# Optimization experiments

Hardware: AMD Instinct MI355X
Metric: run time of the kernel (lower is better)

## Reference

```python
import jax, jax.numpy as jnp
import numpy as np

MARGIN = 0.5
HIERARCHY_LEVEL = 0
EPS = 1e-05


def setup_inputs() -> dict:
    key = jax.random.key(0)
    k1, k2, k3, k4 = jax.random.split(key, 4)
    n, m, d, L, n_classes = 4096, 32768, 128, 2, 100
    embeddings = jax.random.normal(k1, (n, d), dtype=jnp.float32)
    ref_embeddings = jax.random.normal(k2, (m, d), dtype=jnp.float32)
    labels = jax.random.randint(k3, (n, L), 0, n_classes, dtype=jnp.int64)
    ref_labels = jax.random.randint(k4, (m, L), 0, n_classes, dtype=jnp.int64)
    return {"embeddings": embeddings, "labels": labels,
            "ref_embeddings": ref_embeddings, "ref_labels": ref_labels}


def reference(embeddings, labels, ref_embeddings, ref_labels):
    # select hierarchy level
    lab = labels[:, HIERARCHY_LEVEL]          # [n]
    ref_lab = ref_labels[:, HIERARCHY_LEVEL]  # [m]
    n = embeddings.shape[0]
    sim = embeddings @ ref_embeddings.T       # [n, m]
    same = lab[:, None] == ref_lab[None, :]   # [n, m] bool
    # positive pairs: same label and sim < 1 - eps -> contribute (1 - sim)
    pos_mask = same & (sim < 1.0 - EPS)
    # negative pairs: different label and sim > margin -> contribute sim
    neg_mask = (~same) & (sim > MARGIN)
    pos_loss = jnp.sum(jnp.where(pos_mask, 1.0 - sim, 0.0))
    neg_loss = jnp.sum(jnp.where(neg_mask, sim, 0.0))
    return (pos_loss + neg_loss) / n
```

## Files before the change

kernel.cpp:

```cpp
#include <hip/hip_runtime.h>
#include <stdint.h>

#define N_EMB 4096
#define M_REF 32768
#define D_K   128
#define BM    128
#define BN    64
#define NT_PER 16
#define COLCHUNK (BN * NT_PER)
#define NCCHUNK (M_REF / COLCHUNK)
#define NROWT  (N_EMB / BM)
#define XBLOCKS (NROWT * NCCHUNK)

typedef __attribute__((ext_vector_type(8))) short short8;
typedef __attribute__((ext_vector_type(4))) float float4v;

static __device__ __forceinline__ unsigned short f2bf(float f) {
    unsigned int u = __builtin_bit_cast(unsigned int, f);
    u += 0x7FFFu + ((u >> 16) & 1u);
    return (unsigned short)(u >> 16);
}

#define CVT_THREADS (768 * 256)

__global__ void cvt_kernel(const float* __restrict__ emb, const float* __restrict__ ref,
                           unsigned short* __restrict__ aw, unsigned short* __restrict__ bw,
                           float* __restrict__ out) {
    const int NA4 = N_EMB * D_K / 4;
    int i0 = blockIdx.x * 256 + threadIdx.x;
    if (i0 == 0) *out = 0.0f;
    #pragma unroll
    for (int k = 0; k < 6; ++k) {
        int i = i0 + k * CVT_THREADS;
        const float4* src;
        unsigned short* dst;
        int j;
        if (i < NA4) { src = (const float4*)emb; dst = aw; j = i; }
        else         { src = (const float4*)ref; dst = bw; j = i - NA4; }
        float4 v = src[j];
        ushort4 o;
        o.x = f2bf(v.x); o.y = f2bf(v.y); o.z = f2bf(v.z); o.w = f2bf(v.w);
        *(ushort4*)(dst + (size_t)j * 4) = o;
    }
}

static __device__ __forceinline__ void gld_lds16(const void* g, void* l) {
    __builtin_amdgcn_global_load_lds((__attribute__((address_space(1))) void*)g,
                                     (__attribute__((address_space(3))) void*)l,
                                     16, 0, 0);
}

template<int NI>
static __device__ __forceinline__ void stage_rows(const unsigned short* __restrict__ g,
                                                  unsigned short* l, int tid) {
    const int rlow = tid >> 4;
    const int sc   = (tid & 15) ^ rlow;
    const char* g0 = (const char*)g + (rlow * D_K + sc * 8) * 2;
    char* l0 = (char*)l + tid * 16;
    #pragma unroll
    for (int i = 0; i < NI; ++i)
        gld_lds16(g0 + (size_t)i * (16 * D_K * 2), l0 + i * 4096);
}

__launch_bounds__(256, 3)
__global__ void xbm_kernel(const unsigned short* __restrict__ aw,
                           const unsigned short* __restrict__ bw,
                           const int* __restrict__ lab,
                           const int* __restrict__ rlab,
                           float* __restrict__ out) {
    __shared__ unsigned short b_sm[2][BN * D_K];
    __shared__ float red_sm[4];

    const int tid  = threadIdx.x;
    const int lane = tid & 63;
    const int wave = tid >> 6;
    const int quad = lane >> 4;
    const int l15  = lane & 15;

    const int rtile  = blockIdx.x >> 5;
    const int cchunk = blockIdx.x & 31;
    const int row0 = rtile * BM;
    const int col0 = cchunk * COLCHUNK;

    stage_rows<8>(aw + (size_t)row0 * D_K, &b_sm[0][0], tid);

    int labv[2][4];
    #pragma unroll
    for (int mt = 0; mt < 2; ++mt)
        #pragma unroll
        for (int r = 0; r < 4; ++r)
            labv[mt][r] = lab[(row0 + wave * 32 + mt * 16 + quad * 4 + r) * 2];

    __syncthreads();

    short8 a_reg[2][4];
    #pragma unroll
    for (int mt = 0; mt < 2; ++mt) {
        int ml = wave * 32 + mt * 16 + l15;
        #pragma unroll
        for (int ks = 0; ks < 4; ++ks) {
            int cs = (ks * 4 + quad) ^ l15;
            a_reg[mt][ks] = *(const short8*)(&b_sm[0][0] + (size_t)ml * D_K + cs * 8);
        }
    }
    __syncthreads();

    stage_rows<4>(bw + (size_t)col0 * D_K, b_sm[0], tid);

    float lsum[4] = {0.0f, 0.0f, 0.0f, 0.0f};

    #define COMPUTE_TILE(BP, CBASE)                                               \
        {                                                                         \
            const unsigned short* bp_ = (BP);                                     \
            const int cb_ = (CBASE);                                              \
            int rl[4];                                                            \
            _Pragma("unroll")                                                     \
            for (int nt = 0; nt < 4; ++nt)                                        \
                rl[nt] = rlab[(cb_ + nt * 16 + l15) * 2];                         \
            float4v acc[2][4] = {};                                               \
            _Pragma("unroll")                                                     \
            for (int ks = 0; ks < 4; ++ks) {                                      \
                short8 breg[4];                                                   \
                _Pragma("unroll")                                                 \
                for (int nt = 0; nt < 4; ++nt) {                                  \
                    int nl = nt * 16 + l15;                                       \
                    int cs = (ks * 4 + quad) ^ l15;                               \
                    breg[nt] = *(const short8*)(bp_ + (size_t)nl * D_K + cs * 8); \
                }                                                                 \
                _Pragma("unroll")                                                 \
                for (int mt = 0; mt < 2; ++mt)                                    \
                    _Pragma("unroll")                                             \
                    for (int nt = 0; nt < 4; ++nt)                                \
                        acc[mt][nt] = __builtin_amdgcn_mfma_f32_16x16x32_bf16(    \
                            a_reg[mt][ks], breg[nt], acc[mt][nt], 0, 0, 0);       \
            }                                                                     \
            _Pragma("unroll")                                                     \
            for (int mt = 0; mt < 2; ++mt)                                        \
                _Pragma("unroll")                                                 \
                for (int nt = 0; nt < 4; ++nt)                                    \
                    _Pragma("unroll")                                             \
                    for (int r = 0; r < 4; ++r) {                                 \
                        float s = acc[mt][nt][r];                                 \
                               \
                        float pos = fmaxf(1.0f - s, 0.0f);                        \
                        float neg = (s > 0.5f) ? s : 0.0f;                        \
                        lsum[r] += (labv[mt][r] == rl[nt]) ? pos : neg;           \
                    }                                                             \
        }

    #pragma unroll 1
    for (int t = 0; t < NT_PER; t += 2) {
        __syncthreads();
        stage_rows<4>(bw + (size_t)(col0 + (t + 1) * BN) * D_K, b_sm[1], tid);
        COMPUTE_TILE(b_sm[0], col0 + t * BN);
        __syncthreads();
        if (t + 2 < NT_PER)
            stage_rows<4>(bw + (size_t)(col0 + (t + 2) * BN) * D_K, b_sm[0], tid);
        COMPUTE_TILE(b_sm[1], col0 + (t + 1) * BN);
    }

    float loss = (lsum[0] + lsum[1]) + (lsum[2] + lsum[3]);
    #pragma unroll
    for (int off = 32; off > 0; off >>= 1)
        loss += __shfl_down(loss, off, 64);
    if (lane == 0) red_sm[wave] = loss;
    __syncthreads();
    if (tid == 0) {
        float v = (red_sm[0] + red_sm[1] + red_sm[2] + red_sm[3]) * (1.0f / (float)N_EMB);
        atomicAdd(out, v);
    }
}

extern "C" void kernel_launch(void* const* d_in, const int* in_sizes, int n_in,
                              void* d_out, int out_size, void* d_ws, size_t ws_size,
                              hipStream_t stream) {
    const float* emb     = (const float*)d_in[0];
    const int*   labels  = (const int*)d_in[1];
    const float* ref     = (const float*)d_in[2];
    const int*   rlabels = (const int*)d_in[3];
    float* out = (float*)d_out;

    unsigned short* aw = (unsigned short*)d_ws;
    unsigned short* bw = aw + (size_t)N_EMB * D_K;

    cvt_kernel<<<768, 256, 0, stream>>>(emb, ref, aw, bw, out);
    xbm_kernel<<<XBLOCKS, 256, 0, stream>>>(aw, bw,
                                            (const int*)labels, (const int*)rlabels, out);
}
```

Baseline: 120.3 us.

## Restructure GEMM-loss kernel with 4-stage LDS ring and 8-wave 2x4 tiling

Moves to 512-thread blocks with a 2x4 wave grid, each wave holding 64 A rows in registers loaded straight from global memory. B tiles and their labels stream through a 4-deep LDS ring using async global-to-LDS loads with explicit vmcnt waits and raw barriers. Row labels are packed into bytes and MFMA bursts run at raised priority. Fewer, larger blocks with longer column chunks are meant to hide load latency and cut per-block overhead, at the cost of more LDS, tighter register budgets and fragile hand-tuned wait counts.

Measured after the change: 268.2 us. 2.23x slower.

```diff
diff --git a/kernel.cpp b/kernel.cpp
--- a/kernel.cpp
+++ b/kernel.cpp
@@ -6,11 +6,9 @@
 #define D_K   128
 #define BM    128
 #define BN    64
-#define NT_PER 16
-#define COLCHUNK (BN * NT_PER)
-#define NCCHUNK (M_REF / COLCHUNK)
-#define NROWT  (N_EMB / BM)
-#define XBLOCKS (NROWT * NCCHUNK)
+#define NT    32
+#define COLCHUNK (BN * NT)
+#define XBLOCKS ((N_EMB / BM) * (M_REF / COLCHUNK))
 
 typedef __attribute__((ext_vector_type(8))) short short8;
 typedef __attribute__((ext_vector_type(4))) float float4v;
@@ -49,115 +47,139 @@
                                      (__attribute__((address_space(3))) void*)l,
                                      16, 0, 0);
 }
-
-template<int NI>
-static __device__ __forceinline__ void stage_rows(const unsigned short* __restrict__ g,
-                                                  unsigned short* l, int tid) {
-    const int rlow = tid >> 4;
-    const int sc   = (tid & 15) ^ rlow;
-    const char* g0 = (const char*)g + (rlow * D_K + sc * 8) * 2;
-    char* l0 = (char*)l + tid * 16;
-    #pragma unroll
-    for (int i = 0; i < NI; ++i)
-        gld_lds16(g0 + (size_t)i * (16 * D_K * 2), l0 + i * 4096);
-}
-
-__launch_bounds__(256, 3)
+static __device__ __forceinline__ void gld_lds4(const void* g, void* l) {
+    __builtin_amdgcn_global_load_lds((__attribute__((address_space(1))) void*)g,
+                                     (__attribute__((address_space(3))) void*)l,
+                                     4, 0, 0);
+}
+
+#define WAITVM(N) asm volatile("s_waitcnt vmcnt(" #N ")" ::: "memory")
+#define FENCE()   asm volatile("" ::: "memory")
+
+__launch_bounds__(512, 4)
 __global__ void xbm_kernel(const unsigned short* __restrict__ aw,
                            const unsigned short* __restrict__ bw,
                            const int* __restrict__ lab,
                            const int* __restrict__ rlab,
                            float* __restrict__ out) {
-    __shared__ unsigned short b_sm[2][BN * D_K];
-    __shared__ float red_sm[4];
+    __shared__ __align__(16) unsigned short b_sm[4][BN * D_K];
+    __shared__ int lab_sm[4][BN];
+    __shared__ float red_sm[8];
 
     const int tid  = threadIdx.x;
     const int lane = tid & 63;
     const int wave = tid >> 6;
+    const int wm   = wave >> 2;
+    const int wn   = wave & 3;
     const int quad = lane >> 4;
     const int l15  = lane & 15;
 
-    const int rtile  = blockIdx.x >> 5;
-    const int cchunk = blockIdx.x & 31;
+    const int rtile  = blockIdx.x >> 4;
+    const int cchunk = blockIdx.x & 15;
     const int row0 = rtile * BM;
     const int col0 = cchunk * COLCHUNK;
 
-    stage_rows<8>(aw + (size_t)row0 * D_K, &b_sm[0][0], tid);
-
-    int labv[2][4];
-    #pragma unroll
-    for (int mt = 0; mt < 2; ++mt)
+    short8 a_reg[4][4];
+    #pragma unroll
+    for (int mt = 0; mt < 4; ++mt)
         #pragma unroll
-        for (int r = 0; r < 4; ++r)
-            labv[mt][r] = lab[(row0 + wave * 32 + mt * 16 + quad * 4 + r) * 2];
-
-    __syncthreads();
-
-    short8 a_reg[2][4];
-    #pragma unroll
-    for (int mt = 0; mt < 2; ++mt) {
-        int ml = wave * 32 + mt * 16 + l15;
-        #pragma unroll
-        for (int ks = 0; ks < 4; ++ks) {
-            int cs = (ks * 4 + quad) ^ l15;
-            a_reg[mt][ks] = *(const short8*)(&b_sm[0][0] + (size_t)ml * D_K + cs * 8);
+        for (int ks = 0; ks < 4; ++ks)
+            a_reg[mt][ks] = *(const short8*)(aw +
+                (size_t)(row0 + wm * 64 + mt * 16 + l15) * D_K + (ks * 4 + quad) * 8);
+
+    unsigned int labp[4];
+    #pragma unroll
+    for (int mt = 0; mt < 4; ++mt) {
+        int base = (row0 + wm * 64 + mt * 16 + quad * 4) * 2;
+        int4 p0 = *(const int4*)(lab + base);
+        int4 p1 = *(const int4*)(lab + base + 4);
+        labp[mt] = (unsigned)p0.x | ((unsigned)p0.z << 8) |
+                   ((unsigned)p1.x << 16) | ((unsigned)p1.z << 24);
+    }
+
+    #define STAGE(T, R)                                                          \
+        {                                                                        \
+            const char* g0_ = (const char*)(bw + (size_t)(col0 + (T) * BN) * D_K) + \
+                ((tid >> 4) * D_K + (((tid & 15) ^ ((tid >> 4) & 15)) * 8)) * 2; \
+            char* l0_ = (char*)&b_sm[R][0] + tid * 16;                           \
+            gld_lds16(g0_, l0_);                                                 \
+            gld_lds16(g0_ + 32 * 256, l0_ + 8192);                               \
+            gld_lds4(rlab + (size_t)(col0 + (T) * BN + lane) * 2,                \
+                     (char*)&lab_sm[R][0] + lane * 4);                           \
         }
-    }
-    __syncthreads();
-
-    stage_rows<4>(bw + (size_t)col0 * D_K, b_sm[0], tid);
+
+    FENCE();
+    STAGE(0, 0); FENCE();
+    STAGE(1, 1); FENCE();
+    STAGE(2, 2); FENCE();
 
     float lsum[4] = {0.0f, 0.0f, 0.0f, 0.0f};
 
-    #define COMPUTE_TILE(BP, CBASE)                                               \
-        {                                                                         \
-            const unsigned short* bp_ = (BP);                                     \
-            const int cb_ = (CBASE);                                              \
-            int rl[4];                                                            \
-            _Pragma("unroll")                                                     \
-            for (int nt = 0; nt < 4; ++nt)                                        \
-                rl[nt] = rlab[(cb_ + nt * 16 + l15) * 2];                         \
-            float4v acc[2][4] = {};                                               \
-            _Pragma("unroll")                                                     \
-            for (int ks = 0; ks < 4; ++ks) {                                      \
-                short8 breg[4];                                                   \
-                _Pragma("unroll")                                                 \
-                for (int nt = 0; nt < 4; ++nt) {                                  \
-                    int nl = nt * 16 + l15;                                       \
-                    int cs = (ks * 4 + quad) ^ l15;                               \
-                    breg[nt] = *(const short8*)(bp_ + (size_t)nl * D_K + cs * 8); \
-                }                                                                 \
-                _Pragma("unroll")                                                 \
-                for (int mt = 0; mt < 2; ++mt)                                    \
-                    _Pragma("unroll")                                             \
-                    for (int nt = 0; nt < 4; ++nt)                                \
-                        acc[mt][nt] = __builtin_amdgcn_mfma_f32_16x16x32_bf16(    \
-                            a_reg[mt][ks], breg[nt], acc[mt][nt], 0, 0, 0);       \
-            }                                                                     \
-            _Pragma("unroll")                                                     \
-            for (int mt = 0; mt < 2; ++mt)                                        \
-                _Pragma("unroll")                                                 \
-                for (int nt = 0; nt < 4; ++nt)                                    \
-                    _Pragma("unroll")                                             \
-                    for (int r = 0; r < 4; ++r) {                                 \
-                        float s = acc[mt][nt][r];                                 \
-                               \
-                        float pos = fmaxf(1.0f - s, 0.0f);                        \
-                        float neg = (s > 0.5f) ? s : 0.0f;                        \
-                        lsum[r] += (labv[mt][r] == rl[nt]) ? pos : neg;           \
-                    }                                                             \
+    const int bo0 = (wn * 16 + l15) * 256 + ((quad ^ l15) * 16);
+    const int rloff = wn * 16 + l15;
+
+    #define MF(AC, MT, B) AC = __builtin_amdgcn_mfma_f32_16x16x32_bf16(a_reg[MT][0], B, AC, 0, 0, 0)
+
+    #define EPI(A, MT, RL)                                                       \
+        _Pragma("unroll")                                                        \
+        for (int r = 0; r < 4; ++r) {                                            \
+            float s = (A)[r];                                                    \
+            int labr = (int)((labp[MT] >> (r * 8)) & 0xffu);                     \
+                                      \
+            float pos = fmaxf(1.0f - s, 0.0f);                                   \
+            float neg = (s > 0.5f) ? s : 0.0f;                                   \
+            lsum[r] += (labr == (RL)) ? pos : neg;                               \
         }
 
+    #define COMPUTE(R)                                                           \
+        {                                                                        \
+            int rl = lab_sm[R][rloff];                                           \
+            const char* bp_ = (const char*)&b_sm[R][0];                          \
+            short8 b0 = *(const short8*)(bp_ + bo0);                             \
+            short8 b1 = *(const short8*)(bp_ + (bo0 ^ 64));                      \
+            short8 b2 = *(const short8*)(bp_ + (bo0 ^ 128));                     \
+            short8 b3 = *(const short8*)(bp_ + (bo0 ^ 192));                     \
+            float4v a0 = {}, a1 = {}, a2 = {}, a3 = {};                          \
+            __builtin_amdgcn_s_setprio(1);                                       \
+            a0 = __builtin_amdgcn_mfma_f32_16x16x32_bf16(a_reg[0][0], b0, a0, 0, 0, 0); \
+            a1 = __builtin_amdgcn_mfma_f32_16x16x32_bf16(a_reg[1][0], b0, a1, 0, 0, 0); \
+            a2 = __builtin_amdgcn_mfma_f32_16x16x32_bf16(a_reg[2][0], b0, a2, 0, 0, 0); \
+            a3 = __builtin_amdgcn_mfma_f32_16x16x32_bf16(a_reg[3][0], b0, a3, 0, 0, 0); \
+            a0 = __builtin_amdgcn_mfma_f32_16x16x32_bf16(a_reg[0][1], b1, a0, 0, 0, 0); \
+            a1 = __builtin_amdgcn_mfma_f32_16x16x32_bf16(a_reg[1][1], b1, a1, 0, 0, 0); \
+            a2 = __builtin_amdgcn_mfma_f32_16x16x32_bf16(a_reg[2][1], b1, a2, 0, 0, 0); \
+            a3 = __builtin_amdgcn_mfma_f32_16x16x32_bf16(a_reg[3][1], b1, a3, 0, 0, 0); \
+            a0 = __builtin_amdgcn_mfma_f32_16x16x32_bf16(a_reg[0][2], b2, a0, 0, 0, 0); \
+            a1 = __builtin_amdgcn_mfma_f32_16x16x32_bf16(a_reg[1][2], b2, a1, 0, 0, 0); \
+            a2 = __builtin_amdgcn_mfma_f32_16x16x32_bf16(a_reg[2][2], b2, a2, 0, 0, 0); \
+            a3 = __builtin_amdgcn_mfma_f32_16x16x32_bf16(a_reg[3][2], b2, a3, 0, 0, 0); \
+            a0 = __builtin_amdgcn_mfma_f32_16x16x32_bf16(a_reg[0][3], b3, a0, 0, 0, 0); \
+            a1 = __builtin_amdgcn_mfma_f32_16x16x32_bf16(a_reg[1][3], b3, a1, 0, 0, 0); \
+            a2 = __builtin_amdgcn_mfma_f32_16x16x32_bf16(a_reg[2][3], b3, a2, 0, 0, 0); \
+            a3 = __builtin_amdgcn_mfma_f32_16x16x32_bf16(a_reg[3][3], b3, a3, 0, 0, 0); \
+            __builtin_amdgcn_s_setprio(0);                                       \
+            EPI(a0, 0, rl); EPI(a1, 1, rl); EPI(a2, 2, rl); EPI(a3, 3, rl);      \
+        }
+
+    #define ITER_S(T, R, VM)                                                     \
+        WAITVM(VM); __builtin_amdgcn_s_barrier(); FENCE();                       \
+        STAGE((T) + 3, ((R) + 3) & 3);                                           \
+        COMPUTE(R);
+    #define ITER_N(R, VM)                                                        \
+        WAITVM(VM); __builtin_amdgcn_s_barrier(); FENCE();                       \
+        COMPUTE(R);
+
     #pragma unroll 1
-    for (int t = 0; t < NT_PER; t += 2) {
-        __syncthreads();
-        stage_rows<4>(bw + (size_t)(col0 + (t + 1) * BN) * D_K, b_sm[1], tid);
-        COMPUTE_TILE(b_sm[0], col0 + t * BN);
-        __syncthreads();
-        if (t + 2 < NT_PER)
-            stage_rows<4>(bw + (size_t)(col0 + (t + 2) * BN) * D_K, b_sm[0], tid);
-        COMPUTE_TILE(b_sm[1], col0 + (t + 1) * BN);
-    }
+    for (int t0 = 0; t0 < NT - 4; t0 += 4) {
+        ITER_S(t0 + 0, 0, 6);
+        ITER_S(t0 + 1, 1, 6);
+        ITER_S(t0 + 2, 2, 6);
+        ITER_S(t0 + 3, 3, 6);
+    }
+    ITER_S(28, 0, 6);
+    ITER_N(1, 6);
+    ITER_N(2, 3);
+    ITER_N(3, 0);
 
     float loss = (lsum[0] + lsum[1]) + (lsum[2] + lsum[3]);
     #pragma unroll
@@ -166,8 +188,9 @@
     if (lane == 0) red_sm[wave] = loss;
     __syncthreads();
     if (tid == 0) {
-        float v = (red_sm[0] + red_sm[1] + red_sm[2] + red_sm[3]) * (1.0f / (float)N_EMB);
-        atomicAdd(out, v);
+        float v = ((red_sm[0] + red_sm[1]) + (red_sm[2] + red_sm[3])) +
+                  ((red_sm[4] + red_sm[5]) + (red_sm[6] + red_sm[7]));
+        atomicAdd(out, v * (1.0f / (float)N_EMB));
     }
 }
 
@@ -184,6 +207,6 @@
     unsigned short* bw = aw + (size_t)N_EMB * D_K;
 
     cvt_kernel<<<768, 256, 0, stream>>>(emb, ref, aw, bw, out);
-    xbm_kernel<<<XBLOCKS, 256, 0, stream>>>(aw, bw,
+    xbm_kernel<<<XBLOCKS, 512, 0, stream>>>(aw, bw,
                                             (const int*)labels, (const int*)rlabels, out);
 }
```
